# Optimization experiments

Hardware: AMD Instinct MI355X
Metric: run time of the kernel (lower is better)

## Reference

```python
import jax, jax.numpy as jnp
import numpy as np

B, S, D, H = 4, 2048, 1024, 16

def setup_inputs() -> dict:
    key = jax.random.key(0)
    ks = jax.random.split(key, 8)
    s = D ** -0.5
    return {
        "query": jax.random.normal(ks[0], (B, S, D), jnp.float32),
        "bias": jnp.zeros((B, 1, 1, S), jnp.float32),
        "Wq": jax.random.normal(ks[1], (D, D), jnp.float32) * s,
        "bq": jnp.zeros((D,), jnp.float32),
        "Wk": jax.random.normal(ks[2], (D, D), jnp.float32) * s,
        "bk": jnp.zeros((D,), jnp.float32),
        "Wv": jax.random.normal(ks[3], (D, D), jnp.float32) * s,
        "bv": jnp.zeros((D,), jnp.float32),
        "Wo": jax.random.normal(ks[4], (D, D), jnp.float32) * s,
        "bo": jnp.zeros((D,), jnp.float32),
        "leaky_k": jax.random.normal(ks[5], (1, 1, D), jnp.float32) * s,
        "leaky_v": jax.random.normal(ks[6], (1, 1, D), jnp.float32) * s,
    }

def _split_heads(x, heads):
    b, l, c = x.shape
    return x.reshape(b, l, heads, c // heads).transpose(0, 2, 1, 3)  # [b,h,l,dh]

def reference(query, bias, Wq, bq, Wk, bk, Wv, bv, Wo, bo, leaky_k, leaky_v):
    q = query @ Wq.T + bq
    k = query @ Wk.T + bk
    v = query @ Wv.T + bv
    b = query.shape[0]
    # prepend leaky sink key/value token
    k = jnp.concatenate([jnp.broadcast_to(leaky_k, (b, 1, D)), k], axis=1)
    v = jnp.concatenate([jnp.broadcast_to(leaky_v, (b, 1, D)), v], axis=1)
    qh = _split_heads(q, H) * (D // H) ** -0.5
    kh = _split_heads(k, H)
    vh = _split_heads(v, H)
    logits = jnp.einsum('bhqd,bhkd->bhqk', qh, kh)
    # pad bias with zero column for the sink token
    bias_l = jnp.concatenate([jnp.zeros(bias.shape[:3] + (1,), bias.dtype), bias], axis=-1)
    logits = logits + bias_l
    weights = jax.nn.softmax(logits, axis=-1)
    x = jnp.einsum('bhqk,bhkd->bhqd', weights, vh)
    out = x.transpose(0, 2, 1, 3).reshape(b, -1, D)
    return out @ Wo.T + bo
```

## Files before the change

### kernel.cpp

```cpp
#include <hip/hip_runtime.h>
#include <cstdint>
#include <cstddef>

#define DEV static __device__ __forceinline__

typedef __attribute__((ext_vector_type(8))) __bf16 bf16x8;
typedef __attribute__((ext_vector_type(8))) unsigned short u16x8;
typedef __attribute__((ext_vector_type(4))) float f32x4;

#define BB 4
#define SS 2048
#define DD 1024
#define HH 16
#define DH 64
#define SK 2049
#define LOG2E 1.4426950408889634f

DEV unsigned short f2bf(float f) {
  unsigned int u = __builtin_bit_cast(unsigned int, f);
  u += 0x7fffu + ((u >> 16) & 1u);
  return (unsigned short)(u >> 16);
}
DEV float bf2f(unsigned short h) {
  unsigned int u = ((unsigned int)h) << 16;
  return __builtin_bit_cast(float, u);
}

DEV void gl_lds16(const void* g, void* l) {
  __builtin_amdgcn_global_load_lds(
      (const __attribute__((address_space(1))) void*)g,
      (__attribute__((address_space(3))) void*)l, 16, 0, 0);
}

DEV f32x4 mfma_bf16(bf16x8 a, bf16x8 b, f32x4 c) {
  return __builtin_amdgcn_mfma_f32_16x16x32_bf16(a, b, c, 0, 0, 0);
}

__global__ __launch_bounds__(256) void k_convert_query(const float* __restrict__ src,
                                                       unsigned short* __restrict__ dst) {
  int i = blockIdx.x * 256 + threadIdx.x;
  float4 v = reinterpret_cast<const float4*>(src)[i];
  ushort4 o;
  o.x = f2bf(v.x); o.y = f2bf(v.y); o.z = f2bf(v.z); o.w = f2bf(v.w);
  reinterpret_cast<ushort4*>(dst)[i] = o;
}

__global__ __launch_bounds__(256) void k_convert_w(const float* __restrict__ w0,
                                                   const float* __restrict__ w1,
                                                   const float* __restrict__ w2,
                                                   const float* __restrict__ w3,
                                                   unsigned short* __restrict__ wqkv,
                                                   unsigned short* __restrict__ wo) {
  int i = blockIdx.x * 256 + threadIdx.x;
  int e = i * 4;
  int sec = e >> 20;
  int off = e & 1048575;
  const float* s = (sec == 0) ? w0 : (sec == 1) ? w1 : (sec == 2) ? w2 : w3;
  float4 v = *reinterpret_cast<const float4*>(s + off);
  ushort4 o;
  o.x = f2bf(v.x); o.y = f2bf(v.y); o.z = f2bf(v.z); o.w = f2bf(v.w);
  unsigned short* d = (sec < 3) ? (wqkv + (size_t)sec * 1048576 + off) : (wo + off);
  *reinterpret_cast<ushort4*>(d) = o;
}

__global__ __launch_bounds__(256) void k_sink(const float* __restrict__ lk,
                                              const float* __restrict__ lv,
                                              unsigned short* __restrict__ Kh,
                                              unsigned short* __restrict__ Vh) {
  int t = blockIdx.x * 256 + threadIdx.x;
  int bh = t >> 6, d = t & 63;
  int h = bh & (HH - 1);
  Kh[(size_t)bh * SK * DH + d] = f2bf(lk[h * DH + d]);
  Vh[(size_t)bh * SK * DH + d] = f2bf(lv[h * DH + d]);
}


__global__ __launch_bounds__(256) void k_gemm_qkv(const unsigned short* __restrict__ A,
                                                  const unsigned short* __restrict__ Bw,
                                                  const float* __restrict__ bq,
                                                  const float* __restrict__ bk,
                                                  const float* __restrict__ bv,
                                                  unsigned short* __restrict__ Qh,
                                                  unsigned short* __restrict__ Kh,
                                                  unsigned short* __restrict__ Vh) {
  __shared__ unsigned short As[128 * 32];
  __shared__ unsigned short Bs[128 * 32];
  const int tid = threadIdx.x, lane = tid & 63, wid = tid >> 6;
  const int g = lane >> 4, l15 = lane & 15;
  const int m0 = blockIdx.x * 128, n0 = blockIdx.y * 128;
  const int wr = (wid >> 1) * 64, wc = (wid & 1) * 64;

  f32x4 acc[4][4] = {};

  for (int k0 = 0; k0 < 1024; k0 += 32) {
    __syncthreads();
#pragma unroll
    for (int i = 0; i < 2; ++i) {
      int e = i * 2048 + wid * 512 + lane * 8;
      int r = e >> 5, c = e & 31;
      gl_lds16(A + (size_t)(m0 + r) * 1024 + k0 + c, &As[i * 2048 + wid * 512]);
      gl_lds16(Bw + (size_t)(n0 + r) * 1024 + k0 + c, &Bs[i * 2048 + wid * 512]);
    }
    __syncthreads();
    bf16x8 af[4], bf[4];
#pragma unroll
    for (int m = 0; m < 4; ++m)
      af[m] = *reinterpret_cast<const bf16x8*>(&As[(wr + m * 16 + l15) * 32 + g * 8]);
#pragma unroll
    for (int n = 0; n < 4; ++n)
      bf[n] = *reinterpret_cast<const bf16x8*>(&Bs[(wc + n * 16 + l15) * 32 + g * 8]);
#pragma unroll
    for (int m = 0; m < 4; ++m)
#pragma unroll
      for (int n = 0; n < 4; ++n)
        acc[m][n] = mfma_bf16(af[m], bf[n], acc[m][n]);
  }

#pragma unroll
  for (int n = 0; n < 4; ++n) {
    int gn = n0 + wc + n * 16 + l15;
    int sec = gn >> 10;
    int nh = gn & 1023;
    int h = nh >> 6, d = nh & 63;
    const float* bias = (sec == 0) ? bq : (sec == 1) ? bk : bv;
    float bia = bias[nh];
#pragma unroll
    for (int m = 0; m < 4; ++m) {
#pragma unroll
      for (int j = 0; j < 4; ++j) {
        int row = m0 + wr + m * 16 + g * 4 + j;
        int b = row >> 11, s = row & 2047;
        float v = acc[m][n][j] + bia;
        if (sec == 0) {
          Qh[((size_t)(b * HH + h) * SS + s) * DH + d] = f2bf(v * (0.125f * LOG2E));
        } else if (sec == 1) {
          Kh[((size_t)(b * HH + h) * SK + s + 1) * DH + d] = f2bf(v);
        } else {
          Vh[((size_t)(b * HH + h) * SK + s + 1) * DH + d] = f2bf(v);
        }
      }
    }
  }
}

__global__ __launch_bounds__(256) void k_gemm_out(const unsigned short* __restrict__ A,
                                                  const unsigned short* __restrict__ Bw,
                                                  const float* __restrict__ bo,
                                                  float* __restrict__ out) {
  __shared__ unsigned short As[128 * 32];
  __shared__ unsigned short Bs[128 * 32];
  const int tid = threadIdx.x, lane = tid & 63, wid = tid >> 6;
  const int g = lane >> 4, l15 = lane & 15;
  const int m0 = blockIdx.x * 128, n0 = blockIdx.y * 128;
  const int wr = (wid >> 1) * 64, wc = (wid & 1) * 64;

  f32x4 acc[4][4] = {};

  for (int k0 = 0; k0 < 1024; k0 += 32) {
    __syncthreads();
#pragma unroll
    for (int i = 0; i < 2; ++i) {
      int e = i * 2048 + wid * 512 + lane * 8;
      int r = e >> 5, c = e & 31;
      gl_lds16(A + (size_t)(m0 + r) * 1024 + k0 + c, &As[i * 2048 + wid * 512]);
      gl_lds16(Bw + (size_t)(n0 + r) * 1024 + k0 + c, &Bs[i * 2048 + wid * 512]);
    }
    __syncthreads();
    bf16x8 af[4], bf[4];
#pragma unroll
    for (int m = 0; m < 4; ++m)
      af[m] = *reinterpret_cast<const bf16x8*>(&As[(wr + m * 16 + l15) * 32 + g * 8]);
#pragma unroll
    for (int n = 0; n < 4; ++n)
      bf[n] = *reinterpret_cast<const bf16x8*>(&Bs[(wc + n * 16 + l15) * 32 + g * 8]);
#pragma unroll
    for (int m = 0; m < 4; ++m)
#pragma unroll
      for (int n = 0; n < 4; ++n)
        acc[m][n] = mfma_bf16(af[m], bf[n], acc[m][n]);
  }

#pragma unroll
  for (int n = 0; n < 4; ++n) {
    int gn = n0 + wc + n * 16 + l15;
    float bia = bo[gn];
#pragma unroll
    for (int m = 0; m < 4; ++m) {
#pragma unroll
      for (int j = 0; j < 4; ++j) {
        int row = m0 + wr + m * 16 + g * 4 + j;
        out[(size_t)row * 1024 + gn] = acc[m][n][j] + bia;
      }
    }
  }
}

__global__ __launch_bounds__(256) void k_attn(const unsigned short* __restrict__ Qh,
                                              const unsigned short* __restrict__ Kh,
                                              const unsigned short* __restrict__ Vh,
                                              const float* __restrict__ bias,
                                              unsigned short* __restrict__ Xbf) {
  __shared__ unsigned short K_lds[2][64 * 64];
  __shared__ unsigned short VT[2][64 * 64];
  __shared__ unsigned short P_lds[4][16 * 64];

  const int tid = threadIdx.x, lane = tid & 63, w = tid >> 6;
  const int g = lane >> 4, c = lane & 15;
  const int idx = blockIdx.x;
  const int bh = idx >> 4, qt = idx & 15;
  const int b = bh >> 4, h = bh & 15;
  const int q0 = qt * 128 + w * 32;
  const size_t kvbase = (size_t)bh * SK * DH;
  const size_t bbase = (size_t)b * SS;

  bf16x8 qf[2][2];
#pragma unroll
  for (int f = 0; f < 2; ++f)
#pragma unroll
    for (int t = 0; t < 2; ++t)
      qf[f][t] = *reinterpret_cast<const bf16x8*>(
          Qh + ((size_t)bh * SS + q0 + f * 16) * DH + (size_t)c * DH + t * 32 + g * 8);

  bf16x8 kb_sink[2];
#pragma unroll
  for (int t = 0; t < 2; ++t)
    kb_sink[t] = *reinterpret_cast<const bf16x8*>(Kh + kvbase + t * 32 + g * 8);
  float l_sink[2][4], lpart[2][4];
  f32x4 o[2][4];
#pragma unroll
  for (int f = 0; f < 2; ++f) {
    f32x4 s0 = {0.f, 0.f, 0.f, 0.f};
#pragma unroll
    for (int t = 0; t < 2; ++t) s0 = mfma_bf16(qf[f][t], kb_sink[t], s0);
#pragma unroll
    for (int j = 0; j < 4; ++j) {
      l_sink[f][j] = __builtin_amdgcn_exp2f(s0[j]);
      lpart[f][j] = 0.f;
    }
  }
#pragma unroll
  for (int n = 0; n < 4; ++n) {
    float v = bf2f(Vh[kvbase + n * 16 + c]);
#pragma unroll
    for (int f = 0; f < 2; ++f)
#pragma unroll
      for (int j = 0; j < 4; ++j) o[f][n][j] = l_sink[f][j] * v;
  }

  const int kp = tid >> 3;
  const int d0 = (tid & 7) * 8;
  u16x8 pv0, pv1;

  auto stage_k = [&](int key0, unsigned short* Kdst) {
#pragma unroll
    for (int i = 0; i < 2; ++i) {
      int ob = i * 4096 + w * 1024 + lane * 16;
      int r = ob >> 7, cb = ob & 127;
      int sc = cb ^ ((r & 7) << 4);
      gl_lds16(Kh + kvbase + (size_t)(key0 + r + 1) * DH + (sc >> 1),
               (char*)Kdst + i * 4096 + w * 1024);
    }
  };
  auto load_v = [&](int key0) {
    pv0 = *reinterpret_cast<const u16x8*>(Vh + kvbase + (size_t)(key0 + kp * 2 + 1) * DH + d0);
    pv1 = *reinterpret_cast<const u16x8*>(Vh + kvbase + (size_t)(key0 + kp * 2 + 2) * DH + d0);
  };
  auto write_v = [&](unsigned short* VTdst) {
#pragma unroll
    for (int j = 0; j < 8; ++j) {
      int d = d0 + j;
      unsigned int pk = (unsigned int)pv0[j] | ((unsigned int)pv1[j] << 16);
      int byte = (d * 128 + kp * 4) ^ ((j ^ ((d >> 3) & 7)) << 4);
      *(unsigned int*)((char*)VTdst + byte) = pk;
    }
  };

  auto compute_tile = [&](int key0, const unsigned short* Kc, const unsigned short* Vc) {
    float bia[4];
#pragma unroll
    for (int n = 0; n < 4; ++n)
      bia[n] = bias[bbase + key0 + n * 16 + c] * LOG2E;

    f32x4 s[2][4];
    __builtin_amdgcn_s_setprio(1);
#pragma unroll
    for (int n = 0; n < 4; ++n) {
      f32x4 z = {0.f, 0.f, 0.f, 0.f};
      s[0][n] = z; s[1][n] = z;
#pragma unroll
      for (int t = 0; t < 2; ++t) {
        int row = n * 16 + c;
        int byte = (row * 128 + t * 64 + g * 16) ^ ((row & 7) << 4);
        bf16x8 kb = *reinterpret_cast<const bf16x8*>((const char*)Kc + byte);
        s[0][n] = mfma_bf16(qf[0][t], kb, s[0][n]);
        s[1][n] = mfma_bf16(qf[1][t], kb, s[1][n]);
      }
    }
    __builtin_amdgcn_s_setprio(0);

    unsigned short* Pw = P_lds[w];
    bf16x8 pa[2][2];
#pragma unroll
    for (int f = 0; f < 2; ++f) {
#pragma unroll
      for (int n = 0; n < 4; ++n)
#pragma unroll
        for (int j = 0; j < 4; ++j) {
          float p = __builtin_amdgcn_exp2f(s[f][n][j] + bia[n]);
          lpart[f][j] += p;
          int row = g * 4 + j;
          int byte = (row * 128 + (n * 16 + c) * 2) ^ ((row & 7) << 4);
          *(__bf16*)((char*)Pw + byte) = (__bf16)p;
        }
#pragma unroll
      for (int t = 0; t < 2; ++t) {
        int byte = (c * 128 + t * 64 + g * 16) ^ ((c & 7) << 4);
        pa[f][t] = *reinterpret_cast<const bf16x8*>((char*)Pw + byte);
      }
    }

    __builtin_amdgcn_s_setprio(1);
#pragma unroll
    for (int n = 0; n < 4; ++n) {
#pragma unroll
      for (int t = 0; t < 2; ++t) {
        int rv = n * 16 + c;
        int byte = (rv * 128 + t * 64 + g * 16) ^ (((rv & 7) ^ ((rv >> 3) & 7)) << 4);
        bf16x8 vb = *reinterpret_cast<const bf16x8*>((const char*)Vc + byte);
        o[0][n] = mfma_bf16(pa[0][t], vb, o[0][n]);
        o[1][n] = mfma_bf16(pa[1][t], vb, o[1][n]);
      }
    }
    __builtin_amdgcn_s_setprio(0);
  };

  stage_k(0, K_lds[0]);
  load_v(0);
  write_v(VT[0]);
  __syncthreads();

  for (int kt = 0; kt < 32; kt += 2) {
    stage_k((kt + 1) * 64, K_lds[1]);
    load_v((kt + 1) * 64);
    compute_tile(kt * 64, K_lds[0], VT[0]);
    write_v(VT[1]);
    __syncthreads();

    if (kt + 2 < 32) {
      stage_k((kt + 2) * 64, K_lds[0]);
      load_v((kt + 2) * 64);
    }
    compute_tile((kt + 1) * 64, K_lds[1], VT[1]);
    if (kt + 2 < 32) write_v(VT[0]);
    __syncthreads();
  }

#pragma unroll
  for (int mask = 1; mask < 16; mask <<= 1)
#pragma unroll
    for (int f = 0; f < 2; ++f)
#pragma unroll
      for (int j = 0; j < 4; ++j)
        lpart[f][j] += __shfl_xor(lpart[f][j], mask, 64);

#pragma unroll
  for (int f = 0; f < 2; ++f)
#pragma unroll
    for (int j = 0; j < 4; ++j) {
      float inv = 1.f / (l_sink[f][j] + lpart[f][j]);
      int q = q0 + f * 16 + g * 4 + j;
      size_t base = (bbase + q) * DD + h * DH + c;
#pragma unroll
      for (int n = 0; n < 4; ++n) {
        __bf16 hv = (__bf16)(o[f][n][j] * inv);
        Xbf[base + n * 16] = __builtin_bit_cast(unsigned short, hv);
      }
    }
}

extern "C" void kernel_launch(void* const* d_in, const int* in_sizes, int n_in,
                              void* d_out, int out_size, void* d_ws, size_t ws_size,
                              hipStream_t stream) {
  const float* query = (const float*)d_in[0];
  const float* bias  = (const float*)d_in[1];
  const float* Wq = (const float*)d_in[2];
  const float* bq = (const float*)d_in[3];
  const float* Wk = (const float*)d_in[4];
  const float* bk = (const float*)d_in[5];
  const float* Wv = (const float*)d_in[6];
  const float* bv = (const float*)d_in[7];
  const float* Wo = (const float*)d_in[8];
  const float* bo = (const float*)d_in[9];
  const float* lk = (const float*)d_in[10];
  const float* lv = (const float*)d_in[11];

  char* ws = (char*)d_ws;
  unsigned short* Wqkv = (unsigned short*)(ws);
  unsigned short* Wob  = (unsigned short*)(ws + 6291456);
  unsigned short* Qbf  = (unsigned short*)(ws + 8388608);
  unsigned short* Qh   = (unsigned short*)(ws + 25165824);
  unsigned short* Kh   = (unsigned short*)(ws + 41943040);
  unsigned short* Vh   = (unsigned short*)(ws + 58728448);
  unsigned short* Xbf  = Qbf;
  float* out = (float*)d_out;

  k_convert_query<<<8192, 256, 0, stream>>>(query, Qbf);
  k_convert_w<<<4096, 256, 0, stream>>>(Wq, Wk, Wv, Wo, Wqkv, Wob);
  k_sink<<<16, 256, 0, stream>>>(lk, lv, Kh, Vh);
  dim3 g1(64, 24);
  k_gemm_qkv<<<g1, 256, 0, stream>>>(Qbf, Wqkv, bq, bk, bv, Qh, Kh, Vh);
  k_attn<<<1024, 256, 0, stream>>>(Qh, Kh, Vh, bias, Xbf);
  dim3 g2(64, 8);
  k_gemm_out<<<g2, 256, 0, stream>>>(Xbf, Wob, bo, out);
}
```

Measured before the change: 337.2 us.

## Fuse prologue kernels, remap blocks per XCD, prefetch scaled bias into accumulators

Merges the query, weight and sink conversion kernels into one prologue launch that also writes a bias pre-scaled by log2e. The GEMM and attention grids are remapped so consecutive tiles land on the same XCD (id&7 interleave), aiming for better L2 reuse. Attention now prefetches the bias one tile ahead and uses it as the initial MFMA accumulator, removing the per-element add. It also adds a launch_bounds occupancy hint of 4 blocks. The costs are an extra workspace buffer and possible register pressure from the occupancy hint.

```diff
diff --git a/kernel.cpp b/kernel.cpp
--- a/kernel.cpp
+++ b/kernel.cpp
@@ -36,42 +36,47 @@
   return __builtin_amdgcn_mfma_f32_16x16x32_bf16(a, b, c, 0, 0, 0);
 }
 
-__global__ __launch_bounds__(256) void k_convert_query(const float* __restrict__ src,
-                                                       unsigned short* __restrict__ dst) {
-  int i = blockIdx.x * 256 + threadIdx.x;
-  float4 v = reinterpret_cast<const float4*>(src)[i];
-  ushort4 o;
-  o.x = f2bf(v.x); o.y = f2bf(v.y); o.z = f2bf(v.z); o.w = f2bf(v.w);
-  reinterpret_cast<ushort4*>(dst)[i] = o;
-}
-
-__global__ __launch_bounds__(256) void k_convert_w(const float* __restrict__ w0,
-                                                   const float* __restrict__ w1,
-                                                   const float* __restrict__ w2,
-                                                   const float* __restrict__ w3,
-                                                   unsigned short* __restrict__ wqkv,
-                                                   unsigned short* __restrict__ wo) {
-  int i = blockIdx.x * 256 + threadIdx.x;
-  int e = i * 4;
-  int sec = e >> 20;
-  int off = e & 1048575;
-  const float* s = (sec == 0) ? w0 : (sec == 1) ? w1 : (sec == 2) ? w2 : w3;
-  float4 v = *reinterpret_cast<const float4*>(s + off);
-  ushort4 o;
-  o.x = f2bf(v.x); o.y = f2bf(v.y); o.z = f2bf(v.z); o.w = f2bf(v.w);
-  unsigned short* d = (sec < 3) ? (wqkv + (size_t)sec * 1048576 + off) : (wo + off);
-  *reinterpret_cast<ushort4*>(d) = o;
-}
-
-__global__ __launch_bounds__(256) void k_sink(const float* __restrict__ lk,
-                                              const float* __restrict__ lv,
-                                              unsigned short* __restrict__ Kh,
-                                              unsigned short* __restrict__ Vh) {
-  int t = blockIdx.x * 256 + threadIdx.x;
-  int bh = t >> 6, d = t & 63;
-  int h = bh & (HH - 1);
-  Kh[(size_t)bh * SK * DH + d] = f2bf(lk[h * DH + d]);
-  Vh[(size_t)bh * SK * DH + d] = f2bf(lv[h * DH + d]);
+__global__ __launch_bounds__(256) void k_prologue(const float* __restrict__ query,
+                                                  const float* __restrict__ w0,
+                                                  const float* __restrict__ w1,
+                                                  const float* __restrict__ w2,
+                                                  const float* __restrict__ w3,
+                                                  const float* __restrict__ lk,
+                                                  const float* __restrict__ lv,
+                                                  const float* __restrict__ bias,
+                                                  unsigned short* __restrict__ Qbf,
+                                                  unsigned short* __restrict__ wqkv,
+                                                  unsigned short* __restrict__ wo,
+                                                  unsigned short* __restrict__ Kh,
+                                                  unsigned short* __restrict__ Vh,
+                                                  float* __restrict__ biasL) {
+  const int bid = blockIdx.x, tid = threadIdx.x;
+  if (bid < 8192) {
+    int i = bid * 256 + tid;
+    float4 v = reinterpret_cast<const float4*>(query)[i];
+    ushort4 o;
+    o.x = f2bf(v.x); o.y = f2bf(v.y); o.z = f2bf(v.z); o.w = f2bf(v.w);
+    reinterpret_cast<ushort4*>(Qbf)[i] = o;
+  } else if (bid < 12288) {
+    int i = (bid - 8192) * 256 + tid;
+    int e = i * 4;
+    int sec = e >> 20;
+    int off = e & 1048575;
+    const float* s = (sec == 0) ? w0 : (sec == 1) ? w1 : (sec == 2) ? w2 : w3;
+    float4 v = *reinterpret_cast<const float4*>(s + off);
+    ushort4 o;
+    o.x = f2bf(v.x); o.y = f2bf(v.y); o.z = f2bf(v.z); o.w = f2bf(v.w);
+    unsigned short* d = (sec < 3) ? (wqkv + (size_t)sec * 1048576 + off) : (wo + off);
+    *reinterpret_cast<ushort4*>(d) = o;
+  } else {
+    int t = (bid - 12288) * 256 + tid;
+    int bh = t >> 6, d = t & 63;
+    int h = bh & (HH - 1);
+    Kh[(size_t)bh * SK * DH + d] = f2bf(lk[h * DH + d]);
+    Vh[(size_t)bh * SK * DH + d] = f2bf(lv[h * DH + d]);
+    biasL[t] = bias[t] * LOG2E;
+    biasL[t + 4096] = bias[t + 4096] * LOG2E;
+  }
 }
 
 
@@ -87,7 +92,9 @@
   __shared__ unsigned short Bs[128 * 32];
   const int tid = threadIdx.x, lane = tid & 63, wid = tid >> 6;
   const int g = lane >> 4, l15 = lane & 15;
-  const int m0 = blockIdx.x * 128, n0 = blockIdx.y * 128;
+  const int id = blockIdx.x;
+  const int wk = (id & 7) * 192 + (id >> 3);
+  const int m0 = (wk / 24) * 128, n0 = (wk % 24) * 128;
   const int wr = (wid >> 1) * 64, wc = (wid & 1) * 64;
 
   f32x4 acc[4][4] = {};
@@ -151,7 +158,9 @@
   __shared__ unsigned short Bs[128 * 32];
   const int tid = threadIdx.x, lane = tid & 63, wid = tid >> 6;
   const int g = lane >> 4, l15 = lane & 15;
-  const int m0 = blockIdx.x * 128, n0 = blockIdx.y * 128;
+  const int id = blockIdx.x;
+  const int wk = (id & 7) * 64 + (id >> 3);
+  const int m0 = (wk >> 3) * 128, n0 = (wk & 7) * 128;
   const int wr = (wid >> 1) * 64, wc = (wid & 1) * 64;
 
   f32x4 acc[4][4] = {};
@@ -195,18 +204,18 @@
   }
 }
 
-__global__ __launch_bounds__(256) void k_attn(const unsigned short* __restrict__ Qh,
-                                              const unsigned short* __restrict__ Kh,
-                                              const unsigned short* __restrict__ Vh,
-                                              const float* __restrict__ bias,
-                                              unsigned short* __restrict__ Xbf) {
+__global__ __launch_bounds__(256, 4) void k_attn(const unsigned short* __restrict__ Qh,
+                                                 const unsigned short* __restrict__ Kh,
+                                                 const unsigned short* __restrict__ Vh,
+                                                 const float* __restrict__ biasL,
+                                                 unsigned short* __restrict__ Xbf) {
   __shared__ unsigned short K_lds[2][64 * 64];
   __shared__ unsigned short VT[2][64 * 64];
   __shared__ unsigned short P_lds[4][16 * 64];
 
   const int tid = threadIdx.x, lane = tid & 63, w = tid >> 6;
   const int g = lane >> 4, c = lane & 15;
-  const int idx = blockIdx.x;
+  const int idx = (blockIdx.x & 7) * 128 + (blockIdx.x >> 3);
   const int bh = idx >> 4, qt = idx & 15;
   const int b = bh >> 4, h = bh & 15;
   const int q0 = qt * 128 + w * 32;
@@ -265,6 +274,12 @@
     pv0 = *reinterpret_cast<const u16x8*>(Vh + kvbase + (size_t)(key0 + kp * 2 + 1) * DH + d0);
     pv1 = *reinterpret_cast<const u16x8*>(Vh + kvbase + (size_t)(key0 + kp * 2 + 2) * DH + d0);
   };
+  auto load_b = [&](int key0) -> f32x4 {
+    f32x4 r;
+#pragma unroll
+    for (int n = 0; n < 4; ++n) r[n] = biasL[bbase + key0 + n * 16 + c];
+    return r;
+  };
   auto write_v = [&](unsigned short* VTdst) {
 #pragma unroll
     for (int j = 0; j < 8; ++j) {
@@ -275,18 +290,13 @@
     }
   };
 
-  auto compute_tile = [&](int key0, const unsigned short* Kc, const unsigned short* Vc) {
-    float bia[4];
-#pragma unroll
-    for (int n = 0; n < 4; ++n)
-      bia[n] = bias[bbase + key0 + n * 16 + c] * LOG2E;
-
+  auto compute_tile = [&](const unsigned short* Kc, const unsigned short* Vc, f32x4 bR) {
     f32x4 s[2][4];
     __builtin_amdgcn_s_setprio(1);
 #pragma unroll
     for (int n = 0; n < 4; ++n) {
-      f32x4 z = {0.f, 0.f, 0.f, 0.f};
-      s[0][n] = z; s[1][n] = z;
+      f32x4 bi = {bR[n], bR[n], bR[n], bR[n]};
+      s[0][n] = bi; s[1][n] = bi;
 #pragma unroll
       for (int t = 0; t < 2; ++t) {
         int row = n * 16 + c;
@@ -306,7 +316,7 @@
       for (int n = 0; n < 4; ++n)
 #pragma unroll
         for (int j = 0; j < 4; ++j) {
-          float p = __builtin_amdgcn_exp2f(s[f][n][j] + bia[n]);
+          float p = __builtin_amdgcn_exp2f(s[f][n][j]);
           lpart[f][j] += p;
           int row = g * 4 + j;
           int byte = (row * 128 + (n * 16 + c) * 2) ^ ((row & 7) << 4);
@@ -336,21 +346,24 @@
 
   stage_k(0, K_lds[0]);
   load_v(0);
+  f32x4 bA = load_b(0), bB;
   write_v(VT[0]);
   __syncthreads();
 
   for (int kt = 0; kt < 32; kt += 2) {
     stage_k((kt + 1) * 64, K_lds[1]);
     load_v((kt + 1) * 64);
-    compute_tile(kt * 64, K_lds[0], VT[0]);
+    bB = load_b((kt + 1) * 64);
+    compute_tile(K_lds[0], VT[0], bA);
     write_v(VT[1]);
     __syncthreads();
 
     if (kt + 2 < 32) {
       stage_k((kt + 2) * 64, K_lds[0]);
       load_v((kt + 2) * 64);
-    }
-    compute_tile((kt + 1) * 64, K_lds[1], VT[1]);
+      bA = load_b((kt + 2) * 64);
+    }
+    compute_tile(K_lds[1], VT[1], bB);
     if (kt + 2 < 32) write_v(VT[0]);
     __syncthreads();
   }
@@ -401,15 +414,13 @@
   unsigned short* Qh   = (unsigned short*)(ws + 25165824);
   unsigned short* Kh   = (unsigned short*)(ws + 41943040);
   unsigned short* Vh   = (unsigned short*)(ws + 58728448);
+  float* biasL         = (float*)(ws + 75513856);
   unsigned short* Xbf  = Qbf;
   float* out = (float*)d_out;
 
-  k_convert_query<<<8192, 256, 0, stream>>>(query, Qbf);
-  k_convert_w<<<4096, 256, 0, stream>>>(Wq, Wk, Wv, Wo, Wqkv, Wob);
-  k_sink<<<16, 256, 0, stream>>>(lk, lv, Kh, Vh);
-  dim3 g1(64, 24);
-  k_gemm_qkv<<<g1, 256, 0, stream>>>(Qbf, Wqkv, bq, bk, bv, Qh, Kh, Vh);
-  k_attn<<<1024, 256, 0, stream>>>(Qh, Kh, Vh, bias, Xbf);
-  dim3 g2(64, 8);
-  k_gemm_out<<<g2, 256, 0, stream>>>(Xbf, Wob, bo, out);
-}
+  k_prologue<<<12304, 256, 0, stream>>>(query, Wq, Wk, Wv, Wo, lk, lv, bias,
+                                        Qbf, Wqkv, Wob, Kh, Vh, biasL);
+  k_gemm_qkv<<<1536, 256, 0, stream>>>(Qbf, Wqkv, bq, bk, bv, Qh, Kh, Vh);
+  k_attn<<<1024, 256, 0, stream>>>(Qh, Kh, Vh, biasL, Xbf);
+  k_gemm_out<<<512, 256, 0, stream>>>(Xbf, Wob, bo, out);
+}
```

Result: slower. 787.5 us (+133.6%).
